# Optimization experiments

Hardware: AMD Instinct MI355X
Metric: run time of the kernel (lower is better)

Reference implementation:

```python
import jax, jax.numpy as jnp
import numpy as np
import math

N_HEADS = 8


def _grid_sample_bilinear(x, grid):
    """F.grid_sample(x, grid) with bilinear, zero padding, align_corners=False.
    x: [B,C,H,W], grid: [B,Q,N,2] in [-1,1]. Returns [B,Q,N,C] (channels-last)."""
    B, C, H, W = x.shape
    x_nhwc = jnp.transpose(x, (0, 2, 3, 1))  # [B,H,W,C]
    gx = ((grid[..., 0] + 1.0) * W - 1.0) * 0.5  # [B,Q,N]
    gy = ((grid[..., 1] + 1.0) * H - 1.0) * 0.5
    x0 = jnp.floor(gx)
    y0 = jnp.floor(gy)
    fx = gx - x0
    fy = gy - y0
    x0i = x0.astype(jnp.int32)
    y0i = y0.astype(jnp.int32)
    b_idx = jnp.arange(B)[:, None, None]

    def gather(ix, iy):
        valid = (ix >= 0) & (ix < W) & (iy >= 0) & (iy < H)
        v = x_nhwc[b_idx, jnp.clip(iy, 0, H - 1), jnp.clip(ix, 0, W - 1)]  # [B,Q,N,C]
        return v * valid[..., None].astype(x.dtype)

    w00 = ((1.0 - fx) * (1.0 - fy))[..., None]
    w01 = (fx * (1.0 - fy))[..., None]
    w10 = ((1.0 - fx) * fy)[..., None]
    w11 = (fx * fy)[..., None]
    return (gather(x0i, y0i) * w00 + gather(x0i + 1, y0i) * w01 +
            gather(x0i, y0i + 1) * w10 + gather(x0i + 1, y0i + 1) * w11)


def setup_inputs() -> dict:
    key = jax.random.key(0)
    ks = jax.random.split(key, 9)
    B, Q, N, C, H, W = 16, 1000, 16, 256, 100, 100
    x = jax.random.normal(ks[0], (B, C, H, W), dtype=jnp.float32)
    q = jax.random.normal(ks[1], (B, Q, C), dtype=jnp.float32)
    ref_points = jax.random.uniform(ks[2], (B, Q, N, 2), dtype=jnp.float32,
                                    minval=-1.0, maxval=1.0)
    s = 0.02
    wq = jax.random.normal(ks[3], (C, C), dtype=jnp.float32) * s
    bq = jax.random.normal(ks[4], (C,), dtype=jnp.float32) * s
    wk = jax.random.normal(ks[5], (C, C), dtype=jnp.float32) * s
    bk = jax.random.normal(ks[6], (C,), dtype=jnp.float32) * s
    wv = jax.random.normal(ks[7], (C, C), dtype=jnp.float32) * s
    bv = jax.random.normal(ks[8], (C,), dtype=jnp.float32) * s
    return {"x": x, "q": q, "ref_points": ref_points,
            "wq": wq, "bq": bq, "wk": wk, "bk": bk, "wv": wv, "bv": bv}


def reference(x, q, ref_points, wq, bq, wk, bk, wv, bv):
    B, Q, C = q.shape
    N = ref_points.shape[2]
    nh = N_HEADS
    d = C // nh

    qp = q @ wq.T + bq  # [B,Q,C]
    sampled = _grid_sample_bilinear(x, ref_points)          # [B,Q,N,C]
    s = jnp.transpose(sampled, (0, 2, 1, 3))                # [B,N,Q,C] (matches torch transpose(1,-1))
    k = s @ wk.T + bk                                       # [B,N,Q,C]
    v = s @ wv.T + bv

    # Faithful to torch: contiguous [B,N,Q,C] buffer viewed as (B,Q,N,nh,d)
    k = jnp.reshape(k, (B, Q, N, nh, d)).transpose(0, 1, 3, 2, 4)  # [B,Q,nh,N,d]
    v = jnp.reshape(v, (B, Q, N, nh, d)).transpose(0, 1, 3, 2, 4)
    qh = jnp.reshape(qp, (B, Q, nh, d))                            # [B,Q,nh,d]

    attn = jnp.einsum('bqhd,bqhnd->bqhn', qh, k) / math.sqrt(d)
    attn = jax.nn.softmax(attn, axis=-1)
    out = jnp.einsum('bqhn,bqhnd->bqhd', attn, v)
    return out.reshape(B, Q, C)
```

## Files before the change

kernel.cpp:

```cpp
#include <hip/hip_runtime.h>
#include <math.h>

typedef float f4 __attribute__((ext_vector_type(4)));
typedef _Float16 half8 __attribute__((ext_vector_type(8)));

#define C_DIM 256
#define NH 8
#define HD 32
#define Q_DIM 1000
#define N_PTS 16
#define B_DIM 16
#define H_IMG 100
#define W_IMG 100
#define HW 10000
#define BQ2 2
#define NS 32


__global__ __launch_bounds__(256) void xt_kernel(
    const float* __restrict__ x, _Float16* __restrict__ xt) {
  __shared__ float t[64][65];
  int p0 = blockIdx.x * 64;
  int c0 = blockIdx.y * 64;
  int b = blockIdx.z;
  int tid = threadIdx.x;
  int p4 = tid & 15, cl = tid >> 4;
#pragma unroll
  for (int it = 0; it < 4; ++it) {
    int c = cl + 16 * it;
    int p = p0 + p4 * 4;
    f4 v = {0.f, 0.f, 0.f, 0.f};
    const float* sp = x + ((size_t)b * C_DIM + c0 + c) * HW;
    if (p + 3 < HW) {
      v = *(const f4*)(sp + p);
    } else {
#pragma unroll
      for (int j = 0; j < 4; ++j) if (p + j < HW) v[j] = sp[p + j];
    }
    t[p4 * 4 + 0][c] = v[0];
    t[p4 * 4 + 1][c] = v[1];
    t[p4 * 4 + 2][c] = v[2];
    t[p4 * 4 + 3][c] = v[3];
  }
  __syncthreads();
  int pl = tid >> 2, cq = tid & 3;
  int p = p0 + pl;
  if (p < HW) {
    half8 h0, h1;
#pragma unroll
    for (int j = 0; j < 8; ++j) {
      h0[j] = (_Float16)t[pl][cq * 16 + j];
      h1[j] = (_Float16)t[pl][cq * 16 + 8 + j];
    }
    _Float16* dst = xt + ((size_t)b * HW + p) * C_DIM + c0 + cq * 16;
    *(half8*)dst = h0;
    *(half8*)(dst + 8) = h1;
  }
}

__global__ __launch_bounds__(256) void prep_wqk(
    const float* __restrict__ wq, const float* __restrict__ wk,
    const float* __restrict__ bq, _Float16* __restrict__ WqkT,
    float* __restrict__ qkb) {
  int cp = blockIdx.x;
  int h = blockIdx.y;
  int c = threadIdx.x;
  float acc = 0.f, accb = 0.f;
#pragma unroll 4
  for (int dd = 0; dd < HD; ++dd) {
    float wkv = wk[(size_t)(h * HD + dd) * C_DIM + cp];
    acc += wq[(size_t)(h * HD + dd) * C_DIM + c] * wkv;
    accb += bq[h * HD + dd] * wkv;
  }
  const float s = 0.17677669529663687f;
  WqkT[((size_t)h * C_DIM + cp) * C_DIM + c] = (_Float16)(acc * s);
  if (c == 0) qkb[h * C_DIM + cp] = accb * s;
}

__global__ __launch_bounds__(256) void prep_wv(
    const float* __restrict__ wv, _Float16* __restrict__ wvh) {
  int i = blockIdx.x * 256 + threadIdx.x;
  wvh[i] = (_Float16)wv[i];
}

__global__ __launch_bounds__(256) void qk_kernel(
    const float* __restrict__ q, const _Float16* __restrict__ WqkT,
    const float* __restrict__ qkb, _Float16* __restrict__ qk_g) {
  int tid = threadIdx.x;
  int lane = tid & 63;
  int wid = tid >> 6;
  int mtile = blockIdx.x, cg = blockIdx.y;
  int m = lane & 15, kq = lane >> 4;
  int bqr = mtile * 16 + m;
  half8 af[8];
  const float* qrow = q + (size_t)bqr * C_DIM + kq * 8;
#pragma unroll
  for (int ks = 0; ks < 8; ++ks) {
    f4 v0 = *(const f4*)(qrow + ks * 32);
    f4 v1 = *(const f4*)(qrow + ks * 32 + 4);
    half8 a;
    a[0] = (_Float16)v0[0]; a[1] = (_Float16)v0[1];
    a[2] = (_Float16)v0[2]; a[3] = (_Float16)v0[3];
    a[4] = (_Float16)v1[0]; a[5] = (_Float16)v1[1];
    a[6] = (_Float16)v1[2]; a[7] = (_Float16)v1[3];
    af[ks] = a;
  }
#pragma unroll 1
  for (int t = 0; t < 8; ++t) {
    int ct = cg * 32 + wid * 8 + t;
    int h = ct >> 4, nt = ct & 15;
    int cp = nt * 16 + m;
    const _Float16* brow = WqkT + ((size_t)h * C_DIM + cp) * C_DIM + kq * 8;
    f4 acc = {0.f, 0.f, 0.f, 0.f};
#pragma unroll
    for (int ks = 0; ks < 8; ++ks) {
      half8 bf = *(const half8*)(brow + ks * 32);
      acc = __builtin_amdgcn_mfma_f32_16x16x32_f16(af[ks], bf, acc, 0, 0, 0);
    }
    float qb = qkb[h * C_DIM + cp];
#pragma unroll
    for (int r = 0; r < 4; ++r) {
      int bqo = mtile * 16 + kq * 4 + r;
      qk_g[((size_t)bqo * NH + h) * C_DIM + cp] = (_Float16)(acc[r] + qb);
    }
  }
}

__global__ __launch_bounds__(256) void attn_mfma_kernel(
    const _Float16* __restrict__ xt, const float* __restrict__ ref,
    const _Float16* __restrict__ qk_g, _Float16* __restrict__ pv_g) {
  __shared__ __align__(16) _Float16 samp[NS][264];
  __shared__ __align__(16) _Float16 qks[16][264];
  __shared__ float p_s[16][36];

  int tid = threadIdx.x;
  int q2g = blockIdx.x;
  int b = blockIdx.y;
  int q2_0 = q2g * BQ2;
  int m0 = q2g * NS;

  {
    int pair = tid >> 4;
    int col = (tid & 15) * 16;
    int qq = q2_0 + (pair >> 3);
    int hh = pair & 7;
    const _Float16* src = qk_g + (((size_t)b * Q_DIM + qq) * NH + hh) * C_DIM + col;
    *(half8*)&qks[pair][col] = *(const half8*)src;
    *(half8*)&qks[pair][col + 8] = *(const half8*)(src + 8);
  }

  {
    int s_half = tid >> 5, cl = tid & 31;
    const _Float16* base = xt + (size_t)b * HW * C_DIM + cl * 8;
#pragma unroll 1
    for (int it = 0; it < 4; ++it) {
      int i = it * 8 + s_half;
      int mm = m0 + i;
      int qq = mm % Q_DIM, nn = mm / Q_DIM;
      const float* rp = ref + (((size_t)b * Q_DIM + qq) * N_PTS + nn) * 2;
      float gx = (rp[0] + 1.f) * 50.f - 0.5f;
      float gy = (rp[1] + 1.f) * 50.f - 0.5f;
      float fx0 = floorf(gx), fy0 = floorf(gy);
      float fx = gx - fx0, fy = gy - fy0;
      int ix0 = (int)fx0, iy0 = (int)fy0;
      int ix1 = ix0 + 1, iy1 = iy0 + 1;
      bool x0ok = ix0 >= 0 && ix0 < W_IMG, x1ok = ix1 >= 0 && ix1 < W_IMG;
      bool y0ok = iy0 >= 0 && iy0 < H_IMG, y1ok = iy1 >= 0 && iy1 < H_IMG;
      float acc[8] = {0.f, 0.f, 0.f, 0.f, 0.f, 0.f, 0.f, 0.f};
      if (x0ok && y0ok) {
        half8 v = *(const half8*)(base + (size_t)(iy0 * W_IMG + ix0) * C_DIM);
        float w = (1.f - fx) * (1.f - fy);
#pragma unroll
        for (int j = 0; j < 8; ++j) acc[j] += w * (float)v[j];
      }
      if (x1ok && y0ok) {
        half8 v = *(const half8*)(base + (size_t)(iy0 * W_IMG + ix1) * C_DIM);
        float w = fx * (1.f - fy);
#pragma unroll
        for (int j = 0; j < 8; ++j) acc[j] += w * (float)v[j];
      }
      if (x0ok && y1ok) {
        half8 v = *(const half8*)(base + (size_t)(iy1 * W_IMG + ix0) * C_DIM);
        float w = (1.f - fx) * fy;
#pragma unroll
        for (int j = 0; j < 8; ++j) acc[j] += w * (float)v[j];
      }
      if (x1ok && y1ok) {
        half8 v = *(const half8*)(base + (size_t)(iy1 * W_IMG + ix1) * C_DIM);
        float w = fx * fy;
#pragma unroll
        for (int j = 0; j < 8; ++j) acc[j] += w * (float)v[j];
      }
      half8 o;
#pragma unroll
      for (int j = 0; j < 8; ++j) o[j] = (_Float16)acc[j];
      *(half8*)&samp[i][cl * 8] = o;
    }
  }
  __syncthreads();

  {
    int wid = tid >> 6, lane = tid & 63;
    int m_ = lane & 15, kq = lane >> 4;
    if (wid < 2) {
      f4 d = {0.f, 0.f, 0.f, 0.f};
#pragma unroll
      for (int ks = 0; ks < 8; ++ks) {
        half8 a = *(const half8*)&qks[m_][ks * 32 + kq * 8];
        half8 bfr = *(const half8*)&samp[wid * 16 + m_][ks * 32 + kq * 8];
        d = __builtin_amdgcn_mfma_f32_16x16x32_f16(a, bfr, d, 0, 0, 0);
      }
#pragma unroll
      for (int r = 0; r < 4; ++r) {
        int pair = kq * 4 + r;
        float v = d[r];
        float mx = v;
#pragma unroll
        for (int off = 1; off < 16; off <<= 1) mx = fmaxf(mx, __shfl_xor(mx, off, 16));
        float e = __expf(v - mx);
        float s = e;
#pragma unroll
        for (int off = 1; off < 16; off <<= 1) s += __shfl_xor(s, off, 16);
        if ((pair >> 3) == wid) p_s[pair][wid * 16 + m_] = e / s;
      }
    }
  }
  __syncthreads();

  {
    int chunk = tid & 31, pg = tid >> 5;
    float accA[8] = {0.f, 0.f, 0.f, 0.f, 0.f, 0.f, 0.f, 0.f};
    float accB[8] = {0.f, 0.f, 0.f, 0.f, 0.f, 0.f, 0.f, 0.f};
#pragma unroll 4
    for (int n = 0; n < 16; ++n) {
      half8 s0 = *(const half8*)&samp[n][chunk * 8];
      half8 s1 = *(const half8*)&samp[16 + n][chunk * 8];
      float pA = p_s[pg][n];
      float pB = p_s[pg + 8][16 + n];
#pragma unroll
      for (int j = 0; j < 8; ++j) {
        accA[j] += pA * (float)s0[j];
        accB[j] += pB * (float)s1[j];
      }
    }
    half8 oA, oB;
#pragma unroll
    for (int j = 0; j < 8; ++j) {
      oA[j] = (_Float16)accA[j];
      oB[j] = (_Float16)accB[j];
    }
    _Float16* dst = pv_g + (((size_t)b * Q_DIM + q2_0) * NH + pg) * C_DIM + chunk * 8;
    *(half8*)dst = oA;
    *(half8*)(dst + (size_t)NH * C_DIM) = oB;
  }
}

__global__ __launch_bounds__(256) void proj_kernel(
    const _Float16* __restrict__ pv_g, const _Float16* __restrict__ wvh,
    const float* __restrict__ bv, float* __restrict__ out) {
  int tid = threadIdx.x, lane = tid & 63, wid = tid >> 6;
  int mtile = blockIdx.x;
  int m = lane & 15, kq = lane >> 4;
#pragma unroll 1
  for (int hh = 0; hh < 2; ++hh) {
    int h = wid * 2 + hh;
    half8 af[8];
    const _Float16* arow = pv_g + ((size_t)(mtile * 16 + m) * NH + h) * C_DIM + kq * 8;
#pragma unroll
    for (int ks = 0; ks < 8; ++ks) af[ks] = *(const half8*)(arow + ks * 32);
#pragma unroll 1
    for (int nt = 0; nt < 2; ++nt) {
      int c = h * 32 + nt * 16 + m;
      const _Float16* brow = wvh + (size_t)c * C_DIM + kq * 8;
      f4 acc = {0.f, 0.f, 0.f, 0.f};
#pragma unroll
      for (int ks = 0; ks < 8; ++ks)
        acc = __builtin_amdgcn_mfma_f32_16x16x32_f16(af[ks], *(const half8*)(brow + ks * 32),
                                                     acc, 0, 0, 0);
      float bvv = bv[c];
#pragma unroll
      for (int r = 0; r < 4; ++r)
        out[(size_t)(mtile * 16 + kq * 4 + r) * C_DIM + c] = acc[r] + bvv;
    }
  }
}

__global__ __launch_bounds__(256) void transpose_kernel(
    const float* __restrict__ in, float* __restrict__ out, int rows, int cols) {
  __shared__ float t[32][33];
  size_t off = (size_t)blockIdx.z * rows * cols;
  int r0 = blockIdx.y * 32, c0 = blockIdx.x * 32;
  int tx = threadIdx.x, ty = threadIdx.y;
#pragma unroll
  for (int k = 0; k < 4; ++k) {
    int r = r0 + ty + 8 * k, c = c0 + tx;
    if (r < rows && c < cols) t[ty + 8 * k][tx] = in[off + (size_t)r * cols + c];
  }
  __syncthreads();
#pragma unroll
  for (int k = 0; k < 4; ++k) {
    int c = c0 + ty + 8 * k, r = r0 + tx;
    if (r < rows && c < cols) out[off + (size_t)c * rows + r] = t[tx][ty + 8 * k];
  }
}

__global__ __launch_bounds__(256) void qp_kernel(
    const float* __restrict__ q, const float* __restrict__ wq,
    const float* __restrict__ bq, float* __restrict__ qp) {
  __shared__ float qrows[16][257];
  int row0 = blockIdx.x * 16;
  int tid = threadIdx.x;
  for (int t = tid; t < 16 * C_DIM; t += 256) {
    int r = t >> 8, c = t & 255;
    qrows[r][c] = q[(size_t)(row0 + r) * C_DIM + c];
  }
  __syncthreads();
  float acc[16];
  float b0 = bq[tid];
#pragma unroll
  for (int r = 0; r < 16; ++r) acc[r] = b0;
  const float* wrow = wq + (size_t)tid * C_DIM;
  for (int cc = 0; cc < C_DIM; ++cc) {
    float w = wrow[cc];
#pragma unroll
    for (int r = 0; r < 16; ++r) acc[r] += qrows[r][cc] * w;
  }
#pragma unroll
  for (int r = 0; r < 16; ++r) qp[(size_t)(row0 + r) * C_DIM + tid] = acc[r];
}

__global__ __launch_bounds__(256) void attn_fb_kernel(
    const float* __restrict__ src, int strB, int strY, int strX, int strC,
    const float* __restrict__ ref, const float* __restrict__ qp,
    const float* __restrict__ q, const float* __restrict__ wq,
    const float* __restrict__ bq, const float* __restrict__ wk,
    const float* __restrict__ wv, const float* __restrict__ bv,
    float* __restrict__ out) {
  __shared__ __align__(16) float qp_s[BQ2][C_DIM];
  __shared__ __align__(16) float qk_s[16][260];
  __shared__ __align__(16) float samp_f[NS][260];
  __shared__ float p_f[16][16];
  __shared__ float logit_s[256];

  int tid = threadIdx.x;
  int q2g = blockIdx.x;
  int b = blockIdx.y;
  int q2_0 = q2g * BQ2;
  int m0 = q2g * NS;
  int c4 = tid & 63;
  int grp = tid >> 6;

  if (qp) {
    if (tid < 128) {
      int r = tid >> 6, cc4 = tid & 63;
      *(f4*)&qp_s[r][cc4 * 4] =
          *(const f4*)(qp + ((size_t)b * Q_DIM + q2_0 + r) * C_DIM + cc4 * 4);
    }
  } else {
#pragma unroll
    for (int r = 0; r < BQ2; ++r) {
      float acc = bq[tid];
      const float* qrow = q + ((size_t)b * Q_DIM + q2_0 + r) * C_DIM;
      const float* wrow = wq + (size_t)tid * C_DIM;
      for (int cc = 0; cc < C_DIM; ++cc) acc += qrow[cc] * wrow[cc];
      qp_s[r][tid] = acc;
    }
  }

  {
    int coff = tid * strC;
#pragma unroll 1
    for (int i = 0; i < NS; ++i) {
      int mm = m0 + i;
      int qq = mm % Q_DIM;
      int nn = mm / Q_DIM;
      const float* rp = ref + (((size_t)b * Q_DIM + qq) * N_PTS + nn) * 2;
      float gx = (rp[0] + 1.f) * 50.f - 0.5f;
      float gy = (rp[1] + 1.f) * 50.f - 0.5f;
      float fx0 = floorf(gx), fy0 = floorf(gy);
      float fx = gx - fx0, fy = gy - fy0;
      int ix0 = (int)fx0, iy0 = (int)fy0;
      int ix1 = ix0 + 1, iy1 = iy0 + 1;
      float w00 = (1.f - fx) * (1.f - fy);
      float w01 = fx * (1.f - fy);
      float w10 = (1.f - fx) * fy;
      float w11 = fx * fy;
      size_t bse = (size_t)(b * strB + coff);
      float v = 0.f;
      if (ix0 >= 0 && ix0 < W_IMG) {
        if (iy0 >= 0 && iy0 < H_IMG) v += w00 * src[bse + (size_t)iy0 * strY + (size_t)ix0 * strX];
        if (iy1 >= 0 && iy1 < H_IMG) v += w10 * src[bse + (size_t)iy1 * strY + (size_t)ix0 * strX];
      }
      if (ix1 >= 0 && ix1 < W_IMG) {
        if (iy0 >= 0 && iy0 < H_IMG) v += w01 * src[bse + (size_t)iy0 * strY + (size_t)ix1 * strX];
        if (iy1 >= 0 && iy1 < H_IMG) v += w11 * src[bse + (size_t)iy1 * strY + (size_t)ix1 * strX];
      }
      samp_f[i][tid] = v;
    }
  }
  __syncthreads();

#pragma unroll 1
  for (int hh = 0; hh < 2; ++hh) {
    int h = grp * 2 + hh;
    f4 acc0 = {0.f, 0.f, 0.f, 0.f};
    f4 acc1 = {0.f, 0.f, 0.f, 0.f};
#pragma unroll 2
    for (int dd4 = 0; dd4 < 8; ++dd4) {
      f4 a0 = *(const f4*)&qp_s[0][h * HD + dd4 * 4];
      f4 a1 = *(const f4*)&qp_s[1][h * HD + dd4 * 4];
#pragma unroll
      for (int j = 0; j < 4; ++j) {
        f4 w4 = *(const f4*)(wk + (size_t)(h * HD + dd4 * 4 + j) * C_DIM + c4 * 4);
        acc0 += a0[j] * w4;
        acc1 += a1[j] * w4;
      }
    }
    *(f4*)&qk_s[h][c4 * 4] = acc0;
    *(f4*)&qk_s[8 + h][c4 * 4] = acc1;
  }
  __syncthreads();

  {
    int pair = tid >> 4;
    int n2 = tid & 15;
    int i = (pair >> 3) * 16 + n2;
    float acc = 0.f;
#pragma unroll 4
    for (int cc4 = 0; cc4 < 64; ++cc4) {
      f4 qk4 = *(const f4*)&qk_s[pair][cc4 * 4];
      f4 s4 = *(const f4*)&samp_f[i][cc4 * 4];
      acc += qk4[0] * s4[0] + qk4[1] * s4[1] + qk4[2] * s4[2] + qk4[3] * s4[3];
    }
    logit_s[tid] = acc * 0.17677669529663687f;
  }
  __syncthreads();

  if (tid < 16) {
    float mx = -1e30f;
#pragma unroll
    for (int n2 = 0; n2 < 16; ++n2) mx = fmaxf(mx, logit_s[tid * 16 + n2]);
    float s = 0.f;
    float e[16];
#pragma unroll
    for (int n2 = 0; n2 < 16; ++n2) {
      e[n2] = __expf(logit_s[tid * 16 + n2] - mx);
      s += e[n2];
    }
    float inv = 1.f / s;
#pragma unroll
    for (int n2 = 0; n2 < 16; ++n2) p_f[tid][n2] = e[n2] * inv;
  }
  __syncthreads();

#pragma unroll 1
  for (int k = 0; k < 4; ++k) {
    int pair = k * 4 + grp;
    int roff = (pair >> 3) * 16;
    f4 acc = {0.f, 0.f, 0.f, 0.f};
#pragma unroll
    for (int n2 = 0; n2 < 16; ++n2)
      acc += p_f[pair][n2] * *(const f4*)&samp_f[roff + n2][c4 * 4];
    *(f4*)&qk_s[pair][c4 * 4] = acc;
  }
  __syncthreads();

  {
    int h = tid >> 5;
    float acc0 = 0.f, acc1 = 0.f;
#pragma unroll 4
    for (int cc4 = 0; cc4 < 64; ++cc4) {
      f4 pv0 = *(const f4*)&qk_s[h][cc4 * 4];
      f4 pv1 = *(const f4*)&qk_s[8 + h][cc4 * 4];
      f4 w4 = *(const f4*)(wv + (size_t)tid * C_DIM + cc4 * 4);
      acc0 += pv0[0] * w4[0] + pv0[1] * w4[1] + pv0[2] * w4[2] + pv0[3] * w4[3];
      acc1 += pv1[0] * w4[0] + pv1[1] * w4[1] + pv1[2] * w4[2] + pv1[3] * w4[3];
    }
    float bvv = bv[tid];
    out[((size_t)b * Q_DIM + q2_0) * C_DIM + tid] = acc0 + bvv;
    out[((size_t)b * Q_DIM + q2_0 + 1) * C_DIM + tid] = acc1 + bvv;
  }
}

extern "C" void kernel_launch(void* const* d_in, const int* in_sizes, int n_in,
                              void* d_out, int out_size, void* d_ws, size_t ws_size,
                              hipStream_t stream) {
  const float* x   = (const float*)d_in[0];
  const float* q   = (const float*)d_in[1];
  const float* ref = (const float*)d_in[2];
  const float* wq  = (const float*)d_in[3];
  const float* bq  = (const float*)d_in[4];
  const float* wk  = (const float*)d_in[5];
  const float* wv  = (const float*)d_in[7];
  const float* bv  = (const float*)d_in[8];
  float* out = (float*)d_out;

  const size_t XT_B   = (size_t)B_DIM * HW * C_DIM * 2;
  const size_t QK_B   = (size_t)B_DIM * Q_DIM * NH * C_DIM * 2;
  const size_t PV_B   = QK_B;
  const size_t WQKT_B = (size_t)NH * C_DIM * C_DIM * 2;
  const size_t QKB_B  = (size_t)NH * C_DIM * 4;
  const size_t WVH_B  = (size_t)C_DIM * C_DIM * 2;
  const size_t NEED   = XT_B + QK_B + PV_B + WQKT_B + QKB_B + WVH_B;

  if (ws_size >= NEED) {
    char* p = (char*)d_ws;
    _Float16* xt   = (_Float16*)p;            p += XT_B;
    _Float16* qk_g = (_Float16*)p;            p += QK_B;
    _Float16* pv_g = (_Float16*)p;            p += PV_B;
    _Float16* WqkT = (_Float16*)p;            p += WQKT_B;
    float*    qkb  = (float*)p;               p += QKB_B;
    _Float16* wvh  = (_Float16*)p;

    xt_kernel<<<dim3((HW + 63) / 64, C_DIM / 64, B_DIM), 256, 0, stream>>>(x, xt);
    prep_wqk<<<dim3(C_DIM, NH), 256, 0, stream>>>(wq, wk, bq, WqkT, qkb);
    prep_wv<<<C_DIM * C_DIM / 256, 256, 0, stream>>>(wv, wvh);
    qk_kernel<<<dim3(B_DIM * Q_DIM / 16, 4), 256, 0, stream>>>(q, WqkT, qkb, qk_g);
    attn_mfma_kernel<<<dim3(Q_DIM / BQ2, B_DIM), 256, 0, stream>>>(xt, ref, qk_g, pv_g);
    proj_kernel<<<B_DIM * Q_DIM / 16, 256, 0, stream>>>(pv_g, wvh, bv, out);
  } else {
    const size_t QP_BYTES = (size_t)B_DIM * Q_DIM * C_DIM * 4;
    const size_t XTF_BYTES = (size_t)B_DIM * HW * C_DIM * 4;
    float* qp = nullptr;
    float* xtf = nullptr;
    if (ws_size >= QP_BYTES) qp = (float*)d_ws;
    if (ws_size >= QP_BYTES + XTF_BYTES) xtf = (float*)((char*)d_ws + QP_BYTES);

    if (xtf) {
      dim3 g((HW + 31) / 32, C_DIM / 32, B_DIM);
      transpose_kernel<<<g, dim3(32, 8), 0, stream>>>(x, xtf, C_DIM, HW);
    }
    if (qp) qp_kernel<<<B_DIM * Q_DIM / 16, 256, 0, stream>>>(q, wq, bq, qp);

    const float* src;
    int sB, sY, sX, sC;
    if (xtf) { src = xtf; sB = HW * C_DIM; sY = W_IMG * C_DIM; sX = C_DIM; sC = 1; }
    else     { src = x;   sB = C_DIM * HW; sY = W_IMG;         sX = 1;     sC = HW; }

    attn_fb_kernel<<<dim3(Q_DIM / BQ2, B_DIM), 256, 0, stream>>>(
        src, sB, sY, sX, sC, ref, qp, q, wq, bq, wk, wv, bv, out);
  }
}
```

Measured before the change: 561.1 us.

## Replace per-row qk kernel with LDS-tiled 128x128 MFMA GEMM over fp16 q

Measured after the change: 455.5 us. 1.23x faster.

```diff
diff --git a/kernel.cpp b/kernel.cpp
--- a/kernel.cpp
+++ b/kernel.cpp
@@ -15,6 +15,7 @@
 #define HW 10000
 #define BQ2 2
 #define NS 32
+#define N_QK 2048
 
 
 __global__ __launch_bounds__(256) void xt_kernel(
@@ -58,12 +59,25 @@
   }
 }
 
+__global__ __launch_bounds__(256) void qconv_kernel(
+    const float* __restrict__ q, _Float16* __restrict__ qh) {
+  size_t i = ((size_t)blockIdx.x * 256 + threadIdx.x) * 8;
+  f4 v0 = *(const f4*)(q + i);
+  f4 v1 = *(const f4*)(q + i + 4);
+  half8 h;
+  h[0] = (_Float16)v0[0]; h[1] = (_Float16)v0[1];
+  h[2] = (_Float16)v0[2]; h[3] = (_Float16)v0[3];
+  h[4] = (_Float16)v1[0]; h[5] = (_Float16)v1[1];
+  h[6] = (_Float16)v1[2]; h[7] = (_Float16)v1[3];
+  *(half8*)(qh + i) = h;
+}
+
 __global__ __launch_bounds__(256) void prep_wqk(
     const float* __restrict__ wq, const float* __restrict__ wk,
-    const float* __restrict__ bq, _Float16* __restrict__ WqkT,
+    const float* __restrict__ bq, _Float16* __restrict__ wqkB,
     float* __restrict__ qkb) {
-  int cp = blockIdx.x;
-  int h = blockIdx.y;
+  int n = blockIdx.x;
+  int h = n >> 8, cp = n & 255;
   int c = threadIdx.x;
   float acc = 0.f, accb = 0.f;
 #pragma unroll 4
@@ -73,8 +87,8 @@
     accb += bq[h * HD + dd] * wkv;
   }
   const float s = 0.17677669529663687f;
-  WqkT[((size_t)h * C_DIM + cp) * C_DIM + c] = (_Float16)(acc * s);
-  if (c == 0) qkb[h * C_DIM + cp] = accb * s;
+  wqkB[(size_t)n * C_DIM + c] = (_Float16)(acc * s);
+  if (c == 0) qkb[n] = accb * s;
 }
 
 __global__ __launch_bounds__(256) void prep_wv(
@@ -83,46 +97,78 @@
   wvh[i] = (_Float16)wv[i];
 }
 
-__global__ __launch_bounds__(256) void qk_kernel(
-    const float* __restrict__ q, const _Float16* __restrict__ WqkT,
+__global__ __launch_bounds__(256) void qk_gemm(
+    const _Float16* __restrict__ qh, const _Float16* __restrict__ wqkB,
     const float* __restrict__ qkb, _Float16* __restrict__ qk_g) {
+  __shared__ __align__(16) _Float16 lds_buf[2 * 128 * 72];
+  _Float16* As = lds_buf;
+  _Float16* Bs = lds_buf + 128 * 72;
+
   int tid = threadIdx.x;
-  int lane = tid & 63;
-  int wid = tid >> 6;
-  int mtile = blockIdx.x, cg = blockIdx.y;
-  int m = lane & 15, kq = lane >> 4;
-  int bqr = mtile * 16 + m;
-  half8 af[8];
-  const float* qrow = q + (size_t)bqr * C_DIM + kq * 8;
-#pragma unroll
-  for (int ks = 0; ks < 8; ++ks) {
-    f4 v0 = *(const f4*)(qrow + ks * 32);
-    f4 v1 = *(const f4*)(qrow + ks * 32 + 4);
-    half8 a;
-    a[0] = (_Float16)v0[0]; a[1] = (_Float16)v0[1];
-    a[2] = (_Float16)v0[2]; a[3] = (_Float16)v0[3];
-    a[4] = (_Float16)v1[0]; a[5] = (_Float16)v1[1];
-    a[6] = (_Float16)v1[2]; a[7] = (_Float16)v1[3];
-    af[ks] = a;
-  }
-#pragma unroll 1
-  for (int t = 0; t < 8; ++t) {
-    int ct = cg * 32 + wid * 8 + t;
-    int h = ct >> 4, nt = ct & 15;
-    int cp = nt * 16 + m;
-    const _Float16* brow = WqkT + ((size_t)h * C_DIM + cp) * C_DIM + kq * 8;
-    f4 acc = {0.f, 0.f, 0.f, 0.f};
-#pragma unroll
-    for (int ks = 0; ks < 8; ++ks) {
-      half8 bf = *(const half8*)(brow + ks * 32);
-      acc = __builtin_amdgcn_mfma_f32_16x16x32_f16(af[ks], bf, acc, 0, 0, 0);
-    }
-    float qb = qkb[h * C_DIM + cp];
-#pragma unroll
-    for (int r = 0; r < 4; ++r) {
-      int bqo = mtile * 16 + kq * 4 + r;
-      qk_g[((size_t)bqo * NH + h) * C_DIM + cp] = (_Float16)(acc[r] + qb);
-    }
+  int m0 = blockIdx.x * 128;
+  int n0 = blockIdx.y * 128;
+  int wid = tid >> 6, lane = tid & 63;
+  int wm = wid >> 1, wn = wid & 1;
+  int m_ = lane & 15, kq = lane >> 4;
+
+  f4 acc[4][4];
+#pragma unroll
+  for (int i = 0; i < 4; ++i)
+#pragma unroll
+    for (int j = 0; j < 4; ++j) acc[i][j] = {0.f, 0.f, 0.f, 0.f};
+
+#pragma unroll 1
+  for (int k0 = 0; k0 < C_DIM; k0 += 64) {
+    if (k0) __syncthreads();
+#pragma unroll
+    for (int j = 0; j < 4; ++j) {
+      int idx = j * 256 + tid;
+      int r = idx >> 3, kc = idx & 7;
+      *(half8*)&As[r * 72 + kc * 8] =
+          *(const half8*)(qh + (size_t)(m0 + r) * C_DIM + k0 + kc * 8);
+      *(half8*)&Bs[r * 72 + kc * 8] =
+          *(const half8*)(wqkB + (size_t)(n0 + r) * C_DIM + k0 + kc * 8);
+    }
+    __syncthreads();
+#pragma unroll
+    for (int kk = 0; kk < 64; kk += 32) {
+      half8 af[4], bf[4];
+#pragma unroll
+      for (int mt = 0; mt < 4; ++mt)
+        af[mt] = *(const half8*)&As[(wm * 64 + mt * 16 + m_) * 72 + kk + kq * 8];
+#pragma unroll
+      for (int nt = 0; nt < 4; ++nt)
+        bf[nt] = *(const half8*)&Bs[(wn * 64 + nt * 16 + m_) * 72 + kk + kq * 8];
+#pragma unroll
+      for (int mt = 0; mt < 4; ++mt)
+#pragma unroll
+        for (int nt = 0; nt < 4; ++nt)
+          acc[mt][nt] = __builtin_amdgcn_mfma_f32_16x16x32_f16(
+              af[mt], bf[nt], acc[mt][nt], 0, 0, 0);
+    }
+  }
+
+  __syncthreads();
+  _Float16* Cs = lds_buf;
+#pragma unroll
+  for (int nt = 0; nt < 4; ++nt) {
+    int col_l = wn * 64 + nt * 16 + m_;
+    float qb = qkb[n0 + col_l];
+#pragma unroll
+    for (int mt = 0; mt < 4; ++mt) {
+      int row_b = wm * 64 + mt * 16 + kq * 4;
+#pragma unroll
+      for (int r = 0; r < 4; ++r)
+        Cs[(row_b + r) * 136 + col_l] = (_Float16)(acc[mt][nt][r] + qb);
+    }
+  }
+  __syncthreads();
+#pragma unroll
+  for (int j = 0; j < 8; ++j) {
+    int idx = j * 256 + tid;
+    int r = idx >> 4, cc = idx & 15;
+    *(half8*)(qk_g + (size_t)(m0 + r) * N_QK + n0 + cc * 8) =
+        *(const half8*)&Cs[r * 136 + cc * 8];
   }
 }
 
@@ -144,7 +190,7 @@
     int col = (tid & 15) * 16;
     int qq = q2_0 + (pair >> 3);
     int hh = pair & 7;
-    const _Float16* src = qk_g + (((size_t)b * Q_DIM + qq) * NH + hh) * C_DIM + col;
+    const _Float16* src = qk_g + ((size_t)b * Q_DIM + qq) * N_QK + hh * C_DIM + col;
     *(half8*)&qks[pair][col] = *(const half8*)src;
     *(half8*)&qks[pair][col + 8] = *(const half8*)(src + 8);
   }
@@ -495,27 +541,29 @@
   const float* bv  = (const float*)d_in[8];
   float* out = (float*)d_out;
 
-  const size_t XT_B   = (size_t)B_DIM * HW * C_DIM * 2;
-  const size_t QK_B   = (size_t)B_DIM * Q_DIM * NH * C_DIM * 2;
-  const size_t PV_B   = QK_B;
-  const size_t WQKT_B = (size_t)NH * C_DIM * C_DIM * 2;
-  const size_t QKB_B  = (size_t)NH * C_DIM * 4;
-  const size_t WVH_B  = (size_t)C_DIM * C_DIM * 2;
-  const size_t NEED   = XT_B + QK_B + PV_B + WQKT_B + QKB_B + WVH_B;
+  const size_t XT_B    = (size_t)B_DIM * HW * C_DIM * 2;
+  const size_t QK_B    = (size_t)B_DIM * Q_DIM * N_QK * 2;
+  const size_t PV_B    = QK_B;
+  const size_t WQKB_B  = (size_t)N_QK * C_DIM * 2;
+  const size_t QKB_B   = (size_t)N_QK * 4;
+  const size_t WVH_B   = (size_t)C_DIM * C_DIM * 2;
+  const size_t NEED    = XT_B + QK_B + PV_B + WQKB_B + QKB_B + WVH_B;
 
   if (ws_size >= NEED) {
     char* p = (char*)d_ws;
-    _Float16* xt   = (_Float16*)p;            p += XT_B;
-    _Float16* qk_g = (_Float16*)p;            p += QK_B;
-    _Float16* pv_g = (_Float16*)p;            p += PV_B;
-    _Float16* WqkT = (_Float16*)p;            p += WQKT_B;
-    float*    qkb  = (float*)p;               p += QKB_B;
-    _Float16* wvh  = (_Float16*)p;
+    _Float16* xt    = (_Float16*)p;           p += XT_B;
+    _Float16* qk_g  = (_Float16*)p;           p += QK_B;
+    _Float16* pv_g  = (_Float16*)p;           p += PV_B;
+    _Float16* qh    = (_Float16*)pv_g;
+    _Float16* wqkB  = (_Float16*)p;           p += WQKB_B;
+    float*    qkb   = (float*)p;              p += QKB_B;
+    _Float16* wvh   = (_Float16*)p;
 
     xt_kernel<<<dim3((HW + 63) / 64, C_DIM / 64, B_DIM), 256, 0, stream>>>(x, xt);
-    prep_wqk<<<dim3(C_DIM, NH), 256, 0, stream>>>(wq, wk, bq, WqkT, qkb);
+    qconv_kernel<<<(B_DIM * Q_DIM * C_DIM) / (256 * 8), 256, 0, stream>>>(q, qh);
+    prep_wqk<<<N_QK, 256, 0, stream>>>(wq, wk, bq, wqkB, qkb);
     prep_wv<<<C_DIM * C_DIM / 256, 256, 0, stream>>>(wv, wvh);
-    qk_kernel<<<dim3(B_DIM * Q_DIM / 16, 4), 256, 0, stream>>>(q, WqkT, qkb, qk_g);
+    qk_gemm<<<dim3(B_DIM * Q_DIM / 128, N_QK / 128), 256, 0, stream>>>(qh, wqkB, qkb, qk_g);
     attn_mfma_kernel<<<dim3(Q_DIM / BQ2, B_DIM), 256, 0, stream>>>(xt, ref, qk_g, pv_g);
     proj_kernel<<<B_DIM * Q_DIM / 16, 256, 0, stream>>>(pv_g, wvh, bv, out);
   } else {
```
